# Performance work log

Measured on AMD Instinct MI355X. Metric: run time of the kernel, lower is better.

The kernel has to match this reference:

```python
import jax, jax.numpy as jnp
import numpy as np

B, INDIM, POSDIM, L, H, DE, DV, RECEPT = 2, 256, 256, 2048, 8, 64, 64, 64
LN_EPS = 1e-5


def pos_embedding(dim, length):
    # sin/cos with geometric wavelengths length/(0.8 + 1.2**(i+1)); shape (dim, length)
    dsin = dim // 2
    dcos = dim - dsin
    sin_wl = length / (0.8 + 1.2 ** (jnp.arange(dsin, dtype=jnp.float32) + 1.0))[:, None]
    cos_wl = length / (0.8 + 1.2 ** (jnp.arange(dcos, dtype=jnp.float32) + 1.0))[:, None]
    xpos = jnp.arange(length, dtype=jnp.float32)[None, :]
    two_pi = 2.0 * np.pi
    return jnp.concatenate([jnp.sin(two_pi * xpos / sin_wl), jnp.cos(two_pi * xpos / cos_wl)], axis=0)


def _layernorm(x, g, b):
    # normalize over last axis
    mu = jnp.mean(x, axis=-1, keepdims=True)
    var = jnp.mean((x - mu) ** 2, axis=-1, keepdims=True)
    return (x - mu) / jnp.sqrt(var + LN_EPS) * g + b


def setup_inputs() -> dict:
    key = jax.random.key(0)
    ks = jax.random.split(key, 10)
    s = 0.02
    inp = {
        "x": jax.random.normal(ks[0], (B, INDIM, L), dtype=jnp.float32),
        "Wq": jax.random.normal(ks[1], (H * DE, INDIM + POSDIM), dtype=jnp.float32) * s,
        "Wk": jax.random.normal(ks[2], (H * DE, INDIM + POSDIM), dtype=jnp.float32) * s,
        "Wv": jax.random.normal(ks[3], (H * DV, INDIM + POSDIM), dtype=jnp.float32) * s,
        "Wres": jax.random.normal(ks[4], (DV, INDIM), dtype=jnp.float32) * s,
        "Wc": jax.random.normal(ks[5], (DV, H * DV), dtype=jnp.float32) * s,
        "ln1_g": jnp.ones((DV,), jnp.float32),
        "ln1_b": jnp.zeros((DV,), jnp.float32),
        "W1": jax.random.normal(ks[6], (4 * DV, DV), dtype=jnp.float32) * s,
        "W2": jax.random.normal(ks[7], (DV, 4 * DV), dtype=jnp.float32) * s,
        "ln2_g": jnp.ones((DV,), jnp.float32),
        "ln2_b": jnp.zeros((DV,), jnp.float32),
    }
    return inp


def reference(x, Wq, Wk, Wv, Wres, Wc, ln1_g, ln1_b, W1, W2, ln2_g, ln2_b):
    bsz = x.shape[0]
    # residual projection (1x1 conv == channel matmul)
    residual = jnp.einsum('oi,bil->bol', Wres, x)
    # concat positional embedding along channel dim
    pos = pos_embedding(POSDIM, L)
    xp = jnp.concatenate([x, jnp.broadcast_to(pos[None], (bsz,) + pos.shape)], axis=1)
    # QKV projections -> (B, H, D, L)
    q = jnp.einsum('oi,bil->bol', Wq, xp).reshape(bsz, H, DE, L)
    k = jnp.einsum('oi,bil->bol', Wk, xp).reshape(bsz, H, DE, L)
    v = jnp.einsum('oi,bil->bol', Wv, xp).reshape(bsz, H, DV, L)
    # banded receptive attention: mask*(Q^T K); out-of-band scores are exactly 0 (NOT -inf),
    # matching sum(q.unsqueeze(-2) * mask * k.unsqueeze(-3), -1)
    idx = jnp.arange(L)
    band = (jnp.abs(idx[:, None] - idx[None, :]) <= RECEPT).astype(x.dtype)  # (L, L)
    scores = jnp.einsum('bhdl,bhdm->bhlm', q, k) * band / np.float32(np.sqrt(DE))
    attn = jax.nn.softmax(scores, axis=-1)
    # attn @ V^T, back to (B, H, DV, L), flatten heads
    out = jnp.einsum('bhlm,bhvm->bhvl', attn, v).reshape(bsz, H * DV, L)
    pred = jnp.einsum('oi,bil->bol', Wc, out) + residual
    pred = _layernorm(pred.transpose(0, 2, 1), ln1_g, ln1_b).transpose(0, 2, 1)
    # feedforward (1x1 convs) with exact GELU + residual + layernorm
    res2 = pred
    h = jax.nn.gelu(jnp.einsum('oi,bil->bol', W1, pred), approximate=False)
    pred = jnp.einsum('oi,bil->bol', W2, h) + res2
    pred = _layernorm(pred.transpose(0, 2, 1), ln2_g, ln2_b).transpose(0, 2, 1)
    return pred
```

## Files before the change

kernel.cpp:

```cpp
#include <hip/hip_runtime.h>
#include <cstdint>
#include <cstddef>

#define SEQLEN 2048
#define NBATCH 2
#define NIND   256
#define NPOS   256
#define NCIN   512
#define NH     8
#define NDE    64
#define NDV    64
#define NREC   64

typedef __attribute__((ext_vector_type(8))) short s16x8;
typedef __attribute__((ext_vector_type(4))) float f32x4;

__device__ __forceinline__ unsigned short f2bf(float f) {
  union { float f; unsigned u; } v; v.f = f;
  unsigned r = v.u + 0x7fffu + ((v.u >> 16) & 1u);
  return (unsigned short)(r >> 16);
}

__device__ __forceinline__ void gload16(const unsigned short* g, unsigned short* l) {
  __builtin_amdgcn_global_load_lds(
      (const __attribute__((address_space(1))) unsigned int*)g,
      (__attribute__((address_space(3))) unsigned int*)l, 16, 0, 0);
}

__global__ __launch_bounds__(256) void prep_k(const float* __restrict__ x,
                                              const float* __restrict__ Wq,
                                              const float* __restrict__ Wk,
                                              const float* __restrict__ Wv,
                                              const float* __restrict__ Wc,
                                              const float* __restrict__ Wres,
                                              const float* __restrict__ W1,
                                              const float* __restrict__ W2,
                                              unsigned short* __restrict__ xpt,
                                              unsigned short* __restrict__ wqb,
                                              unsigned short* __restrict__ wkb,
                                              unsigned short* __restrict__ wvb,
                                              unsigned short* __restrict__ wcb,
                                              unsigned short* __restrict__ wresb,
                                              unsigned short* __restrict__ w1b,
                                              unsigned short* __restrict__ w2b,
                                              float* __restrict__ vsum) {
  __shared__ float tile[64][65];
  int blk = blockIdx.x;
  int t = threadIdx.x;
  if (blk < 512) {
    int b = blk >> 8, c0 = ((blk >> 5) & 7) * 64, l0 = (blk & 31) * 64;
    if (c0 < NIND) {
      const float* src = x + ((size_t)b * NIND + c0) * SEQLEN;
      int ll = t & 63, cq = t >> 6;
#pragma unroll
      for (int i = 0; i < 16; ++i) {
        int cl = cq * 16 + i;
        tile[cl][ll] = src[(size_t)cl * SEQLEN + l0 + ll];
      }
      __syncthreads();
      int cl2 = t & 63, lq = t >> 6;
      unsigned short* dst = xpt + ((size_t)b * SEQLEN + l0) * NCIN + c0;
#pragma unroll
      for (int i = 0; i < 16; ++i) {
        int l = lq * 16 + i;
        dst[(size_t)l * NCIN + cl2] = f2bf(tile[cl2][l]);
      }
    } else {
      int c = c0 + (t & 63);
      int j = c - NIND;
      int i = (j < NPOS / 2) ? j : j - NPOS / 2;
      const double base = (double)1.2f;
      double p = 1.0;
      for (int tt = 0; tt <= i; ++tt) p *= base;
      float w = 0.8f + (float)p;
      float swl = (float)SEQLEN / w;
      const float two_pi = (float)(2.0 * 3.14159265358979323846);
      int wv = t >> 6;
      unsigned short* dst = xpt + (size_t)b * SEQLEN * NCIN;
#pragma unroll
      for (int it = 0; it < 16; ++it) {
        int l = l0 + 16 * wv + it;
        float arg = (two_pi * (float)l) / swl;
        float val = (j < NPOS / 2) ? sinf(arg) : cosf(arg);
        dst[(size_t)l * NCIN + c] = f2bf(val);
      }
    }
  } else if (blk == 1360) {
    ((float4*)vsum)[t] = make_float4(0.f, 0.f, 0.f, 0.f);
  } else {
    const float* in;
    unsigned short* out;
    int idx4;
    if (blk < 1280) {
      int i = (blk - 512) * 256 + t;
      int which = i >> 16;
      idx4 = i & 65535;
      in = (which == 0) ? Wq : ((which == 1) ? Wk : Wv);
      out = (which == 0) ? wqb : ((which == 1) ? wkb : wvb);
    } else if (blk < 1312) { in = Wc;   out = wcb;   idx4 = (blk - 1280) * 256 + t; }
    else if (blk < 1328)   { in = Wres; out = wresb; idx4 = (blk - 1312) * 256 + t; }
    else if (blk < 1344)   { in = W1;   out = w1b;   idx4 = (blk - 1328) * 256 + t; }
    else                   { in = W2;   out = w2b;   idx4 = (blk - 1344) * 256 + t; }
    float4 v = ((const float4*)in)[idx4];
    ((ushort4*)out)[idx4] = make_ushort4(f2bf(v.x), f2bf(v.y), f2bf(v.z), f2bf(v.w));
  }
}

__global__ __launch_bounds__(256) void qkv_gemm_k(const unsigned short* __restrict__ Wqb,
                                                  const unsigned short* __restrict__ Wkb,
                                                  const unsigned short* __restrict__ Wvb,
                                                  const unsigned short* __restrict__ xpt,
                                                  unsigned short* __restrict__ qt,
                                                  unsigned short* __restrict__ kt,
                                                  unsigned short* __restrict__ vb,
                                                  float* __restrict__ vsum) {
  __shared__ alignas(16) unsigned short lds[12288];
  unsigned short* Al = lds;
  unsigned short* Bl = lds + 4096;

  int bz = blockIdx.z;
  int y = blockIdx.y;
  int ysel = y >> 3;
  int m0 = (y & 7) * 64;
  int n0 = blockIdx.x * 128;
  const unsigned short* W = (ysel == 0) ? Wqb : ((ysel == 1) ? Wkb : Wvb);
  const unsigned short* Bg = xpt + (size_t)bz * SEQLEN * NCIN;

  int t = threadIdx.x;
  int w = t >> 6, lane = t & 63, lr = lane & 15, hi = lane >> 4;
  int wm = w >> 1, wn = w & 1;

  int sr = lane >> 3;
  int scs = ((lane & 7) ^ sr) * 8;
  const unsigned short* gA0 = W  + (size_t)(m0 + 16 * w + sr) * 512 + scs;
  const unsigned short* gB0 = Bg + (size_t)(n0 + 32 * w + sr) * 512 + scs;
  unsigned short* lA0 = &Al[(16 * w) * 64];
  unsigned short* lB0 = &Bl[(32 * w) * 64];

  int swz = (lr & 7) << 3;

  f32x4 acc[2][4];
#pragma unroll
  for (int i = 0; i < 2; ++i)
#pragma unroll
    for (int j = 0; j < 4; ++j) acc[i][j] = (f32x4){0.f, 0.f, 0.f, 0.f};

  for (int k0 = 0; k0 < 512; k0 += 64) {
    __syncthreads();
    gload16(gA0 + k0,            lA0);
    gload16(gA0 + k0 + 8 * 512,  lA0 + 8 * 64);
    gload16(gB0 + k0,            lB0);
    gload16(gB0 + k0 + 8 * 512,  lB0 + 8 * 64);
    gload16(gB0 + k0 + 16 * 512, lB0 + 16 * 64);
    gload16(gB0 + k0 + 24 * 512, lB0 + 24 * 64);
    __syncthreads();
#pragma unroll
    for (int ks = 0; ks < 2; ++ks) {
      s16x8 af[2], bfv[4];
#pragma unroll
      for (int mt = 0; mt < 2; ++mt)
        af[mt] = *(const s16x8*)&Al[(32 * wm + 16 * mt + lr) * 64 + ((32 * ks + 8 * hi) ^ swz)];
#pragma unroll
      for (int nt = 0; nt < 4; ++nt)
        bfv[nt] = *(const s16x8*)&Bl[(64 * wn + 16 * nt + lr) * 64 + ((32 * ks + 8 * hi) ^ swz)];
#pragma unroll
      for (int mt = 0; mt < 2; ++mt)
#pragma unroll
        for (int nt = 0; nt < 4; ++nt)
          acc[mt][nt] = __builtin_amdgcn_mfma_f32_16x16x32_bf16(af[mt], bfv[nt], acc[mt][nt], 0, 0, 0);
    }
  }

  if (ysel == 2) {
#pragma unroll
    for (int mt = 0; mt < 2; ++mt)
#pragma unroll
      for (int reg = 0; reg < 4; ++reg) {
        float p = acc[mt][0][reg] + acc[mt][1][reg] + acc[mt][2][reg] + acc[mt][3][reg];
        p += __shfl_xor(p, 1, 64);
        p += __shfl_xor(p, 2, 64);
        p += __shfl_xor(p, 4, 64);
        p += __shfl_xor(p, 8, 64);
        if (lr == 0)
          atomicAdd(&vsum[bz * 512 + m0 + 32 * wm + 16 * mt + 4 * hi + reg], p);
      }
  }
  __syncthreads();

  if (ysel < 2) {
    unsigned short* Cl = lds;
#pragma unroll
    for (int mt = 0; mt < 2; ++mt)
#pragma unroll
      for (int nt = 0; nt < 4; ++nt) {
        int lloc = 64 * wn + 16 * nt + lr;
        int d0 = 32 * wm + 16 * mt + 4 * hi;
        *(ushort4*)&Cl[lloc * 68 + d0] = make_ushort4(f2bf(acc[mt][nt][0]), f2bf(acc[mt][nt][1]),
                                                      f2bf(acc[mt][nt][2]), f2bf(acc[mt][nt][3]));
      }
    __syncthreads();
    int h = m0 >> 6;
    unsigned short* Cb = ((ysel == 0) ? qt : kt) + ((size_t)(bz * NH + h) * SEQLEN + n0) * 64;
    int rr = t >> 1, cc = (t & 1) * 32;
#pragma unroll
    for (int j = 0; j < 4; ++j)
      *(int4*)&Cb[(size_t)rr * 64 + cc + 8 * j] = *(const int4*)&Cl[rr * 68 + cc + 8 * j];
  } else {
    unsigned short* Cl2 = lds;
#pragma unroll
    for (int mt = 0; mt < 2; ++mt)
#pragma unroll
      for (int nt = 0; nt < 4; ++nt) {
        int lloc = 64 * wn + 16 * nt + lr;
#pragma unroll
        for (int reg = 0; reg < 4; ++reg)
          Cl2[(32 * wm + 16 * mt + 4 * hi + reg) * 132 + lloc] = f2bf(acc[mt][nt][reg]);
      }
    __syncthreads();
    int dd = t >> 2, cc = (t & 3) * 32;
    unsigned short* Vb = vb + ((size_t)(bz * 512 + m0 + dd)) * SEQLEN + n0;
#pragma unroll
    for (int j = 0; j < 4; ++j)
      *(int4*)&Vb[cc + 8 * j] = *(const int4*)&Cl2[dd * 132 + cc + 8 * j];
  }
}

__global__ __launch_bounds__(256) void attn_k(const unsigned short* __restrict__ qt,
                                              const unsigned short* __restrict__ kt,
                                              const unsigned short* __restrict__ vb,
                                              const float* __restrict__ vsum,
                                              unsigned short* __restrict__ attnt) {
  __shared__ alignas(16) unsigned short Ps[64 * 200];
  __shared__ float rowcoef[64];

  int bz = blockIdx.z, hh = blockIdx.y;
  int l0 = blockIdx.x * 64;
  int bh = bz * NH + hh;
  const unsigned short* Qb = qt + (size_t)bh * SEQLEN * 64;
  const unsigned short* Kb = kt + (size_t)bh * SEQLEN * 64;
  const unsigned short* Vp = vb + (size_t)(bz * 512 + hh * 64) * SEQLEN;
  int vsbase = bz * 512 + hh * 64;

  int t = threadIdx.x;
  int w = t >> 6, lane = t & 63, lr = lane & 15, hi = lane >> 4;

  union U { int4 i4; s16x8 v; };

  U a0, a1;
  a0.v = *(const s16x8*)(Qb + ((size_t)(l0 + 16 * w + lr)) * 64 + 8 * hi);
  a1.v = *(const s16x8*)(Qb + ((size_t)(l0 + 16 * w + lr)) * 64 + 32 + 8 * hi);

  f32x4 sc[12];
#pragma unroll
  for (int ct = 0; ct < 12; ++ct) {
    int m = l0 - 64 + 16 * ct + lr;
    U b0, b1;
    b0.i4 = make_int4(0, 0, 0, 0);
    b1.i4 = make_int4(0, 0, 0, 0);
    if (m >= 0 && m < SEQLEN) {
      b0.v = *(const s16x8*)(Kb + (size_t)m * 64 + 8 * hi);
      b1.v = *(const s16x8*)(Kb + (size_t)m * 64 + 32 + 8 * hi);
    }
    f32x4 acc = {0.f, 0.f, 0.f, 0.f};
    acc = __builtin_amdgcn_mfma_f32_16x16x32_bf16(a0.v, b0.v, acc, 0, 0, 0);
    acc = __builtin_amdgcn_mfma_f32_16x16x32_bf16(a1.v, b1.v, acc, 0, 0, 0);
    sc[ct] = acc;
  }

  float rcv[4];
#pragma unroll
  for (int i = 0; i < 4; ++i) {
    int r = 16 * w + 4 * hi + i;
    int l = l0 + r;
    float mx = 0.0f;
    float sv[12];
#pragma unroll
    for (int ct = 0; ct < 12; ++ct) {
      int c = 16 * ct + lr;
      int m = l0 - 64 + c;
      bool ib = (c >= r) && (c <= r + 128) && (m >= 0) && (m < SEQLEN);
      float s = sc[ct][i] * 0.125f;
      sv[ct] = ib ? s : -1e30f;
      mx = ib ? fmaxf(mx, s) : mx;
    }
    mx = fmaxf(mx, __shfl_xor(mx, 1, 64));
    mx = fmaxf(mx, __shfl_xor(mx, 2, 64));
    mx = fmaxf(mx, __shfl_xor(mx, 4, 64));
    mx = fmaxf(mx, __shfl_xor(mx, 8, 64));
    float e0 = expf(-mx);
    float zs = 0.f;
#pragma unroll
    for (int ct = 0; ct < 12; ++ct) {
      float e = (sv[ct] > -1e29f) ? expf(sv[ct] - mx) : 0.0f;
      sv[ct] = e;
      zs += e;
    }
    zs += __shfl_xor(zs, 1, 64);
    zs += __shfl_xor(zs, 2, 64);
    zs += __shfl_xor(zs, 4, 64);
    zs += __shfl_xor(zs, 8, 64);
    int lo = l - NREC; if (lo < 0) lo = 0;
    int hi2 = l + NREC; if (hi2 > SEQLEN - 1) hi2 = SEQLEN - 1;
    float inv = 1.0f / (zs + (float)(SEQLEN - (hi2 - lo + 1)) * e0);
    rcv[i] = e0 * inv;
#pragma unroll
    for (int ct = 0; ct < 12; ++ct)
      sc[ct][i] = (sv[ct] > 0.0f) ? (sv[ct] - e0) * inv : 0.0f;
  }

#pragma unroll
  for (int i = 0; i < 4; ++i) {
    int r = 16 * w + 4 * hi + i;
#pragma unroll
    for (int ct = 0; ct < 12; ++ct)
      Ps[r * 200 + 16 * ct + lr] = f2bf(sc[ct][i]);
  }
  if (lr == 0) {
#pragma unroll
    for (int i = 0; i < 4; ++i) rowcoef[16 * w + 4 * hi + i] = rcv[i];
  }
  __syncthreads();

  U av[6];
#pragma unroll
  for (int ks = 0; ks < 6; ++ks) {
    int m8 = l0 - 64 + 32 * ks + 8 * hi;
    av[ks].i4 = make_int4(0, 0, 0, 0);
    if (m8 >= 0 && m8 < SEQLEN)
      av[ks].v = *(const s16x8*)(Vp + (size_t)(16 * w + lr) * SEQLEN + m8);
  }
  float vsv[4];
#pragma unroll
  for (int reg = 0; reg < 4; ++reg) vsv[reg] = vsum[vsbase + 16 * w + 4 * hi + reg];

  unsigned short* Ob = attnt + ((size_t)bz * SEQLEN) * 512 + hh * 64;
#pragma unroll
  for (int nt = 0; nt < 4; ++nt) {
    f32x4 acc = {0.f, 0.f, 0.f, 0.f};
#pragma unroll
    for (int ks = 0; ks < 6; ++ks) {
      s16x8 b = *(const s16x8*)&Ps[(16 * nt + lr) * 200 + 32 * ks + 8 * hi];
      acc = __builtin_amdgcn_mfma_f32_16x16x32_bf16(av[ks].v, b, acc, 0, 0, 0);
    }
    int l = l0 + 16 * nt + lr;
    float rcf = rowcoef[16 * nt + lr];
    ushort4 o = make_ushort4(f2bf(acc[0] + rcf * vsv[0]), f2bf(acc[1] + rcf * vsv[1]),
                             f2bf(acc[2] + rcf * vsv[2]), f2bf(acc[3] + rcf * vsv[3]));
    *(ushort4*)&Ob[(size_t)l * 512 + 16 * w + 4 * hi] = o;
  }
}

__global__ __launch_bounds__(256) void tail_k(const unsigned short* __restrict__ wcb,
                                              const unsigned short* __restrict__ wresb,
                                              const unsigned short* __restrict__ w1b,
                                              const unsigned short* __restrict__ w2b,
                                              const unsigned short* __restrict__ attnt,
                                              const unsigned short* __restrict__ xpt,
                                              const float* __restrict__ g1v,
                                              const float* __restrict__ b1v,
                                              const float* __restrict__ g2v,
                                              const float* __restrict__ b2v,
                                              float* __restrict__ outp) {
  __shared__ float gs1[64], bs1[64], gs2[64], bs2[64];
  __shared__ alignas(16) unsigned short pw[4][16][72];
  __shared__ alignas(16) unsigned short hw[4][16][264];

  int b = blockIdx.y;
  int l0 = blockIdx.x * 64;
  int t = threadIdx.x, w = t >> 6, lane = t & 63, lr = lane & 15, hi = lane >> 4;
  if (t < 64) { gs1[t] = g1v[t]; bs1[t] = b1v[t]; gs2[t] = g2v[t]; bs2[t] = b2v[t]; }
  __syncthreads();

  int lloc = 16 * w + lr;
  const unsigned short* brow = attnt + ((size_t)b * SEQLEN + l0 + lloc) * 512;
  const unsigned short* xrow = xpt + ((size_t)b * SEQLEN + l0 + lloc) * 512;

  f32x4 acc[4];
#pragma unroll
  for (int i = 0; i < 4; ++i) acc[i] = (f32x4){0.f, 0.f, 0.f, 0.f};
#pragma unroll
  for (int ks = 0; ks < 16; ++ks) {
    s16x8 bf = *(const s16x8*)(brow + 32 * ks + 8 * hi);
#pragma unroll
    for (int mt = 0; mt < 4; ++mt) {
      s16x8 af = *(const s16x8*)(wcb + (size_t)(16 * mt + lr) * 512 + 32 * ks + 8 * hi);
      acc[mt] = __builtin_amdgcn_mfma_f32_16x16x32_bf16(af, bf, acc[mt], 0, 0, 0);
    }
  }
#pragma unroll
  for (int ks = 0; ks < 8; ++ks) {
    s16x8 bf = *(const s16x8*)(xrow + 32 * ks + 8 * hi);
#pragma unroll
    for (int mt = 0; mt < 4; ++mt) {
      s16x8 af = *(const s16x8*)(wresb + (size_t)(16 * mt + lr) * 256 + 32 * ks + 8 * hi);
      acc[mt] = __builtin_amdgcn_mfma_f32_16x16x32_bf16(af, bf, acc[mt], 0, 0, 0);
    }
  }
  float resid[4][4];
  {
    float sum = 0.f, sq = 0.f;
#pragma unroll
    for (int mt = 0; mt < 4; ++mt)
#pragma unroll
      for (int reg = 0; reg < 4; ++reg) { float v = acc[mt][reg]; sum += v; sq += v * v; }
    sum += __shfl_xor(sum, 16, 64); sq += __shfl_xor(sq, 16, 64);
    sum += __shfl_xor(sum, 32, 64); sq += __shfl_xor(sq, 32, 64);
    float mu = sum * (1.0f / 64.0f);
    float var = sq * (1.0f / 64.0f) - mu * mu;
    float rstd = rsqrtf(var + 1e-5f);
#pragma unroll
    for (int mt = 0; mt < 4; ++mt) {
      float o[4];
#pragma unroll
      for (int reg = 0; reg < 4; ++reg) {
        int m = 16 * mt + 4 * hi + reg;
        o[reg] = (acc[mt][reg] - mu) * rstd * gs1[m] + bs1[m];
        resid[mt][reg] = o[reg];
      }
      *(ushort4*)&pw[w][lr][16 * mt + 4 * hi] =
          make_ushort4(f2bf(o[0]), f2bf(o[1]), f2bf(o[2]), f2bf(o[3]));
    }
  }
  __syncthreads();

  {
    s16x8 bf0 = *(const s16x8*)&pw[w][lr][8 * hi];
    s16x8 bf1 = *(const s16x8*)&pw[w][lr][32 + 8 * hi];
#pragma unroll
    for (int mt = 0; mt < 16; ++mt) {
      s16x8 a0 = *(const s16x8*)(w1b + (size_t)(16 * mt + lr) * 64 + 8 * hi);
      s16x8 a1 = *(const s16x8*)(w1b + (size_t)(16 * mt + lr) * 64 + 32 + 8 * hi);
      f32x4 a2 = {0.f, 0.f, 0.f, 0.f};
      a2 = __builtin_amdgcn_mfma_f32_16x16x32_bf16(a0, bf0, a2, 0, 0, 0);
      a2 = __builtin_amdgcn_mfma_f32_16x16x32_bf16(a1, bf1, a2, 0, 0, 0);
      float v0 = a2[0], v1 = a2[1], v2 = a2[2], v3 = a2[3];
      v0 = 0.5f * v0 * (1.0f + erff(v0 * 0.70710678118654752440f));
      v1 = 0.5f * v1 * (1.0f + erff(v1 * 0.70710678118654752440f));
      v2 = 0.5f * v2 * (1.0f + erff(v2 * 0.70710678118654752440f));
      v3 = 0.5f * v3 * (1.0f + erff(v3 * 0.70710678118654752440f));
      *(ushort4*)&hw[w][lr][16 * mt + 4 * hi] = make_ushort4(f2bf(v0), f2bf(v1), f2bf(v2), f2bf(v3));
    }
  }
  __syncthreads();

  f32x4 acc3[4];
#pragma unroll
  for (int i = 0; i < 4; ++i) acc3[i] = (f32x4){0.f, 0.f, 0.f, 0.f};
#pragma unroll
  for (int ks = 0; ks < 8; ++ks) {
    s16x8 bf = *(const s16x8*)&hw[w][lr][32 * ks + 8 * hi];
#pragma unroll
    for (int mt = 0; mt < 4; ++mt) {
      s16x8 af = *(const s16x8*)(w2b + (size_t)(16 * mt + lr) * 256 + 32 * ks + 8 * hi);
      acc3[mt] = __builtin_amdgcn_mfma_f32_16x16x32_bf16(af, bf, acc3[mt], 0, 0, 0);
    }
  }
#pragma unroll
  for (int mt = 0; mt < 4; ++mt)
#pragma unroll
    for (int reg = 0; reg < 4; ++reg) acc3[mt][reg] += resid[mt][reg];
  float sum = 0.f, sq = 0.f;
#pragma unroll
  for (int mt = 0; mt < 4; ++mt)
#pragma unroll
    for (int reg = 0; reg < 4; ++reg) { float v = acc3[mt][reg]; sum += v; sq += v * v; }
  sum += __shfl_xor(sum, 16, 64); sq += __shfl_xor(sq, 16, 64);
  sum += __shfl_xor(sum, 32, 64); sq += __shfl_xor(sq, 32, 64);
  float mu = sum * (1.0f / 64.0f);
  float var = sq * (1.0f / 64.0f) - mu * mu;
  float rstd = rsqrtf(var + 1e-5f);
  float* ob = outp + (size_t)b * 64 * SEQLEN;
  int l = l0 + lloc;
#pragma unroll
  for (int mt = 0; mt < 4; ++mt)
#pragma unroll
    for (int reg = 0; reg < 4; ++reg) {
      int m = 16 * mt + 4 * hi + reg;
      ob[(size_t)m * SEQLEN + l] = (acc3[mt][reg] - mu) * rstd * gs2[m] + bs2[m];
    }
}

extern "C" void kernel_launch(void* const* d_in, const int* in_sizes, int n_in,
                              void* d_out, int out_size, void* d_ws, size_t ws_size,
                              hipStream_t stream) {
  const float* x    = (const float*)d_in[0];
  const float* Wq   = (const float*)d_in[1];
  const float* Wk   = (const float*)d_in[2];
  const float* Wv   = (const float*)d_in[3];
  const float* Wres = (const float*)d_in[4];
  const float* Wc   = (const float*)d_in[5];
  const float* ln1g = (const float*)d_in[6];
  const float* ln1b = (const float*)d_in[7];
  const float* W1   = (const float*)d_in[8];
  const float* W2   = (const float*)d_in[9];
  const float* ln2g = (const float*)d_in[10];
  const float* ln2b = (const float*)d_in[11];

  char* base = (char*)d_ws;
  unsigned short* xpt   = (unsigned short*)base; base += (size_t)2097152 * 2;
  unsigned short* wqb   = (unsigned short*)base; base += (size_t)262144 * 2;
  unsigned short* wkb   = (unsigned short*)base; base += (size_t)262144 * 2;
  unsigned short* wvb   = (unsigned short*)base; base += (size_t)262144 * 2;
  unsigned short* wcb   = (unsigned short*)base; base += (size_t)32768 * 2;
  unsigned short* wresb = (unsigned short*)base; base += (size_t)16384 * 2;
  unsigned short* w1b   = (unsigned short*)base; base += (size_t)16384 * 2;
  unsigned short* w2b   = (unsigned short*)base; base += (size_t)16384 * 2;
  unsigned short* qt    = (unsigned short*)base; base += (size_t)2097152 * 2;
  unsigned short* kt    = (unsigned short*)base; base += (size_t)2097152 * 2;
  unsigned short* vbb   = (unsigned short*)base; base += (size_t)2097152 * 2;
  float* vsum           = (float*)base;          base += (size_t)1024 * 4;
  unsigned short* attnt = (unsigned short*)base; base += (size_t)2097152 * 2;
  float* outp = (float*)d_out;

  prep_k<<<1361, 256, 0, stream>>>(x, Wq, Wk, Wv, Wc, Wres, W1, W2,
                                   xpt, wqb, wkb, wvb, wcb, wresb, w1b, w2b, vsum);
  qkv_gemm_k<<<dim3(16, 24, NBATCH), 256, 0, stream>>>(wqb, wkb, wvb, xpt, qt, kt, vbb, vsum);
  attn_k<<<dim3(32, NH, NBATCH), 256, 0, stream>>>(qt, kt, vbb, vsum, attnt);
  tail_k<<<dim3(32, NBATCH), 256, 0, stream>>>(wcb, wresb, w1b, w2b, attnt, xpt,
                                               ln1g, ln1b, ln2g, ln2b, outp);
}
```

Before: 80.21 us.

## Double-buffer QKV GEMM LDS staging and drop attention edge bounds checks

The QKV GEMM now keeps two LDS buffers and issues the async global-to-LDS loads for the next K-slice while running MFMAs on the current one, leaving one barrier per iteration instead of two. This is meant to hide global load latency in that GEMM. In exchange, LDS per block doubles to 48 KB, which can lower occupancy. Separately, the attention kernel no longer zero-fills K and V fragments at sequence edges and loads them unconditionally, removing branches. Those edge loads can now read outside the current head's data (or before the buffer start), and they rely on masking and zero probabilities to cancel the values, which fails if the neighbouring memory holds NaN or Inf.

```diff
diff --git a/kernel.cpp b/kernel.cpp
--- a/kernel.cpp
+++ b/kernel.cpp
@@ -114,9 +114,7 @@
                                                   unsigned short* __restrict__ kt,
                                                   unsigned short* __restrict__ vb,
                                                   float* __restrict__ vsum) {
-  __shared__ alignas(16) unsigned short lds[12288];
-  unsigned short* Al = lds;
-  unsigned short* Bl = lds + 4096;
+  __shared__ alignas(16) unsigned short lds[24576];
 
   int bz = blockIdx.z;
   int y = blockIdx.y;
@@ -134,8 +132,6 @@
   int scs = ((lane & 7) ^ sr) * 8;
   const unsigned short* gA0 = W  + (size_t)(m0 + 16 * w + sr) * 512 + scs;
   const unsigned short* gB0 = Bg + (size_t)(n0 + 32 * w + sr) * 512 + scs;
-  unsigned short* lA0 = &Al[(16 * w) * 64];
-  unsigned short* lB0 = &Bl[(32 * w) * 64];
 
   int swz = (lr & 7) << 3;
 
@@ -145,30 +141,43 @@
 #pragma unroll
     for (int j = 0; j < 4; ++j) acc[i][j] = (f32x4){0.f, 0.f, 0.f, 0.f};
 
-  for (int k0 = 0; k0 < 512; k0 += 64) {
-    __syncthreads();
-    gload16(gA0 + k0,            lA0);
-    gload16(gA0 + k0 + 8 * 512,  lA0 + 8 * 64);
-    gload16(gB0 + k0,            lB0);
-    gload16(gB0 + k0 + 8 * 512,  lB0 + 8 * 64);
-    gload16(gB0 + k0 + 16 * 512, lB0 + 16 * 64);
-    gload16(gB0 + k0 + 24 * 512, lB0 + 24 * 64);
-    __syncthreads();
+  auto stage = [&](int buf, int k0) {
+    unsigned short* Ad = lds + buf * 12288 + (16 * w) * 64;
+    unsigned short* Bd = lds + buf * 12288 + 4096 + (32 * w) * 64;
+    gload16(gA0 + k0,            Ad);
+    gload16(gA0 + k0 + 8 * 512,  Ad + 8 * 64);
+    gload16(gB0 + k0,            Bd);
+    gload16(gB0 + k0 + 8 * 512,  Bd + 8 * 64);
+    gload16(gB0 + k0 + 16 * 512, Bd + 16 * 64);
+    gload16(gB0 + k0 + 24 * 512, Bd + 24 * 64);
+  };
+  auto compute = [&](int buf) {
+    const unsigned short* Ar = lds + buf * 12288;
+    const unsigned short* Br = Ar + 4096;
 #pragma unroll
     for (int ks = 0; ks < 2; ++ks) {
       s16x8 af[2], bfv[4];
 #pragma unroll
       for (int mt = 0; mt < 2; ++mt)
-        af[mt] = *(const s16x8*)&Al[(32 * wm + 16 * mt + lr) * 64 + ((32 * ks + 8 * hi) ^ swz)];
+        af[mt] = *(const s16x8*)&Ar[(32 * wm + 16 * mt + lr) * 64 + ((32 * ks + 8 * hi) ^ swz)];
 #pragma unroll
       for (int nt = 0; nt < 4; ++nt)
-        bfv[nt] = *(const s16x8*)&Bl[(64 * wn + 16 * nt + lr) * 64 + ((32 * ks + 8 * hi) ^ swz)];
+        bfv[nt] = *(const s16x8*)&Br[(64 * wn + 16 * nt + lr) * 64 + ((32 * ks + 8 * hi) ^ swz)];
 #pragma unroll
       for (int mt = 0; mt < 2; ++mt)
 #pragma unroll
         for (int nt = 0; nt < 4; ++nt)
           acc[mt][nt] = __builtin_amdgcn_mfma_f32_16x16x32_bf16(af[mt], bfv[nt], acc[mt][nt], 0, 0, 0);
     }
+  };
+
+  stage(0, 0);
+  __syncthreads();
+#pragma unroll
+  for (int it = 0; it < 8; ++it) {
+    if (it < 7) stage((it + 1) & 1, (it + 1) * 64);
+    compute(it & 1);
+    __syncthreads();
   }
 
   if (ysel == 2) {
@@ -185,7 +194,6 @@
           atomicAdd(&vsum[bz * 512 + m0 + 32 * wm + 16 * mt + 4 * hi + reg], p);
       }
   }
-  __syncthreads();
 
   if (ysel < 2) {
     unsigned short* Cl = lds;
@@ -244,26 +252,19 @@
   int t = threadIdx.x;
   int w = t >> 6, lane = t & 63, lr = lane & 15, hi = lane >> 4;
 
-  union U { int4 i4; s16x8 v; };
-
-  U a0, a1;
-  a0.v = *(const s16x8*)(Qb + ((size_t)(l0 + 16 * w + lr)) * 64 + 8 * hi);
-  a1.v = *(const s16x8*)(Qb + ((size_t)(l0 + 16 * w + lr)) * 64 + 32 + 8 * hi);
+  s16x8 a0 = *(const s16x8*)(Qb + ((size_t)(l0 + 16 * w + lr)) * 64 + 8 * hi);
+  s16x8 a1 = *(const s16x8*)(Qb + ((size_t)(l0 + 16 * w + lr)) * 64 + 32 + 8 * hi);
 
   f32x4 sc[12];
 #pragma unroll
   for (int ct = 0; ct < 12; ++ct) {
     int m = l0 - 64 + 16 * ct + lr;
-    U b0, b1;
-    b0.i4 = make_int4(0, 0, 0, 0);
-    b1.i4 = make_int4(0, 0, 0, 0);
-    if (m >= 0 && m < SEQLEN) {
-      b0.v = *(const s16x8*)(Kb + (size_t)m * 64 + 8 * hi);
-      b1.v = *(const s16x8*)(Kb + (size_t)m * 64 + 32 + 8 * hi);
-    }
+    const unsigned short* kp = Kb + (ptrdiff_t)m * 64;
+    s16x8 b0 = *(const s16x8*)(kp + 8 * hi);
+    s16x8 b1 = *(const s16x8*)(kp + 32 + 8 * hi);
     f32x4 acc = {0.f, 0.f, 0.f, 0.f};
-    acc = __builtin_amdgcn_mfma_f32_16x16x32_bf16(a0.v, b0.v, acc, 0, 0, 0);
-    acc = __builtin_amdgcn_mfma_f32_16x16x32_bf16(a1.v, b1.v, acc, 0, 0, 0);
+    acc = __builtin_amdgcn_mfma_f32_16x16x32_bf16(a0, b0, acc, 0, 0, 0);
+    acc = __builtin_amdgcn_mfma_f32_16x16x32_bf16(a1, b1, acc, 0, 0, 0);
     sc[ct] = acc;
   }
 
@@ -321,13 +322,11 @@
   }
   __syncthreads();
 
-  U av[6];
+  s16x8 av[6];
 #pragma unroll
   for (int ks = 0; ks < 6; ++ks) {
     int m8 = l0 - 64 + 32 * ks + 8 * hi;
-    av[ks].i4 = make_int4(0, 0, 0, 0);
-    if (m8 >= 0 && m8 < SEQLEN)
-      av[ks].v = *(const s16x8*)(Vp + (size_t)(16 * w + lr) * SEQLEN + m8);
+    av[ks] = *(const s16x8*)(Vp + (ptrdiff_t)(16 * w + lr) * SEQLEN + m8);
   }
   float vsv[4];
 #pragma unroll
@@ -340,7 +339,7 @@
 #pragma unroll
     for (int ks = 0; ks < 6; ++ks) {
       s16x8 b = *(const s16x8*)&Ps[(16 * nt + lr) * 200 + 32 * ks + 8 * hi];
-      acc = __builtin_amdgcn_mfma_f32_16x16x32_bf16(av[ks].v, b, acc, 0, 0, 0);
+      acc = __builtin_amdgcn_mfma_f32_16x16x32_bf16(av[ks], b, acc, 0, 0, 0);
     }
     int l = l0 + 16 * nt + lr;
     float rcf = rowcoef[16 * nt + lr];
```

After: 80.20 us. About the same (-0.0%).
